# Kernel optimization log

Measured on AMD Instinct MI355X. Metric: run time of the kernel, lower is better.

Reference implementation:

```python
import jax, jax.numpy as jnp
import numpy as np

NUM_HEADS = 4
OUTPUT_DIM = 32
NUM_NODES = 50000
NUM_EDGES = 800000
INPUT_DIM = 128


def setup_inputs() -> dict:
    key = jax.random.key(0)
    k1, k2, k3, k4 = jax.random.split(key, 4)
    node_features = jax.random.uniform(k1, (NUM_NODES, INPUT_DIM), dtype=jnp.float32)
    edge_index = jax.random.randint(k2, (2, NUM_EDGES), 0, NUM_NODES, dtype=jnp.int64)
    # Linear weight (xavier-like scale), stored as [in, out] for x @ W
    W = jax.random.normal(k3, (INPUT_DIM, NUM_HEADS * OUTPUT_DIM), dtype=jnp.float32) * 0.1
    att = jax.random.normal(k4, (2 * OUTPUT_DIM, 1), dtype=jnp.float32) * 0.2
    return {"node_features": node_features, "edge_index": edge_index, "W": W, "att": att}


def reference(node_features, edge_index, W, att):
    num_nodes = node_features.shape[0]
    # Linear projection -> [N, H, D]  (dropout = identity in eval mode)
    proj = (node_features @ W).reshape(num_nodes, NUM_HEADS, OUTPUT_DIM)
    src = proj[edge_index[0]]   # [E, H, D]
    tgt = proj[edge_index[1]]   # [E, H, D]
    # concat([src,tgt]) @ att  ==  src @ att[:D] + tgt @ att[D:]
    a_src = att[:OUTPUT_DIM, 0]   # [D]
    a_tgt = att[OUTPUT_DIM:, 0]   # [D]
    scores = jax.nn.leaky_relu(
        jnp.einsum('ehd,d->eh', src, a_src) + jnp.einsum('ehd,d->eh', tgt, a_tgt),
        negative_slope=0.01,
    )  # [E, H]
    # Faithful to original: softmax over the HEADS axis (dim=-1 of [E, H])
    alpha = jax.nn.softmax(scores, axis=-1)  # [E, H]
    weighted = tgt * alpha[..., None]        # [E, H, D]
    # index_add_ on dim 0 with edge_index[0]
    out = jax.ops.segment_sum(weighted, edge_index[0], num_segments=num_nodes)  # [N, H, D]
    # concat_heads=False -> mean over heads
    return out.mean(axis=1)  # [N, D]
```

## Files before the change

kernel.cpp:

```cpp
#include <hip/hip_runtime.h>
#include <math.h>

#define N_NODES 50000
#define N_EDGES 800000
#define IN_DIM 128
#define N_HEADS 4
#define OUT_DIM 32
#define PROJ_DIM 128
#define CAP 48
#define WSTR 144
#define DEGS 16

#define PROJ_BLKS 391
#define BUCKET_BLKS 1563
#define TOTAL_BLKS (PROJ_BLKS + BUCKET_BLKS)

typedef short bf16x8 __attribute__((ext_vector_type(8)));
typedef float f32x4  __attribute__((ext_vector_type(4)));
typedef _Float16 h2  __attribute__((ext_vector_type(2)));

__device__ __forceinline__ ushort f32_to_bf16(float f) {
    unsigned u = __float_as_uint(f);
    unsigned r = u + 0x7fffu + ((u >> 16) & 1u);
    return (ushort)(r >> 16);
}

__device__ __forceinline__ float bf16_to_f32(ushort v) {
    return __uint_as_float((unsigned)v << 16);
}

__device__ __forceinline__ bf16x8 cvt8(float4 a, float4 b) {
    bf16x8 r;
    r[0] = (short)f32_to_bf16(a.x); r[1] = (short)f32_to_bf16(a.y);
    r[2] = (short)f32_to_bf16(a.z); r[3] = (short)f32_to_bf16(a.w);
    r[4] = (short)f32_to_bf16(b.x); r[5] = (short)f32_to_bf16(b.y);
    r[6] = (short)f32_to_bf16(b.z); r[7] = (short)f32_to_bf16(b.w);
    return r;
}

__global__ __launch_bounds__(256) void combo_kernel(
    const float* __restrict__ X, const float* __restrict__ W,
    const float* __restrict__ att, const int* __restrict__ ei,
    ushort* __restrict__ projT, float* __restrict__ s_src, float* __restrict__ s_tgt,
    int* __restrict__ deg, ushort* __restrict__ bucket)
{
    __shared__ ushort Wt[128 * WSTR];

    const int tid = threadIdx.x;

    if (blockIdx.x >= PROJ_BLKS) {
        int b2 = blockIdx.x - PROJ_BLKS;
        int e0 = b2 * 512 + tid;
#pragma unroll
        for (int i = 0; i < 2; ++i) {
            int e = e0 + i * 256;
            if (e < N_EDGES) {
                int src = ei[e];
                int tgt = ei[N_EDGES + e];
                int pos = atomicAdd(&deg[src * DEGS], 1);
                if (pos < CAP)
                    __builtin_nontemporal_store((ushort)tgt, &bucket[src * CAP + pos]);
            }
        }
        return;
    }

    for (int idx = tid; idx < 64 * 128; idx += 256) {
        int kp = idx >> 7;
        int c  = idx & 127;
        float w0 = W[(2 * kp) * PROJ_DIM + c];
        float w1 = W[(2 * kp + 1) * PROJ_DIM + c];
        unsigned pr = (unsigned)f32_to_bf16(w0) | ((unsigned)f32_to_bf16(w1) << 16);
        *(unsigned*)&Wt[c * WSTR + 2 * kp] = pr;
    }
    __syncthreads();

    const int wv   = tid >> 6;
    const int lane = tid & 63;
    const int m = lane & 15;
    const int q = lane >> 4;
    const int rbase = blockIdx.x * 128;

    int arow0 = rbase + wv * 32 + m;
    int arow1 = arow0 + 16;
    arow0 = (arow0 < N_NODES) ? arow0 : N_NODES - 1;
    arow1 = (arow1 < N_NODES) ? arow1 : N_NODES - 1;
    const long long xb0 = (long long)arow0 * IN_DIM;
    const long long xb1 = (long long)arow1 * IN_DIM;

    f32x4 acc[2][8];
#pragma unroll
    for (int rt = 0; rt < 2; ++rt)
#pragma unroll
        for (int ct = 0; ct < 8; ++ct) acc[rt][ct] = (f32x4){0.f, 0.f, 0.f, 0.f};

#pragma unroll
    for (int ks = 0; ks < 4; ++ks) {
        const int k0 = ks * 32 + q * 8;
        float4 a0lo = *(const float4*)&X[xb0 + k0];
        float4 a0hi = *(const float4*)&X[xb0 + k0 + 4];
        float4 a1lo = *(const float4*)&X[xb1 + k0];
        float4 a1hi = *(const float4*)&X[xb1 + k0 + 4];
        bf16x8 afrag0 = cvt8(a0lo, a0hi);
        bf16x8 afrag1 = cvt8(a1lo, a1hi);
#pragma unroll
        for (int ct = 0; ct < 8; ++ct) {
            bf16x8 bfrag = *(const bf16x8*)&Wt[(ct * 16 + m) * WSTR + k0];
            acc[0][ct] = __builtin_amdgcn_mfma_f32_16x16x32_bf16(afrag0, bfrag, acc[0][ct], 0, 0, 0);
            acc[1][ct] = __builtin_amdgcn_mfma_f32_16x16x32_bf16(afrag1, bfrag, acc[1][ct], 0, 0, 0);
        }
    }

    const float as_lo = att[m],      as_hi = att[m + 16];
    const float at_lo = att[32 + m], at_hi = att[48 + m];

#pragma unroll
    for (int rt = 0; rt < 2; ++rt) {
        const int rowb = rbase + wv * 32 + rt * 16 + q * 4;
#pragma unroll
        for (int r = 0; r < 4; ++r) {
            const int row = rowb + r;
            float cl[4], ch[4];
#pragma unroll
            for (int h = 0; h < 4; ++h) {
                cl[h] = acc[rt][2 * h][r];
                ch[h] = acc[rt][2 * h + 1][r];
            }
            if (row < N_NODES) {
                ushort4 plo, phi;
                plo.x = f32_to_bf16(cl[0]); plo.y = f32_to_bf16(cl[1]);
                plo.z = f32_to_bf16(cl[2]); plo.w = f32_to_bf16(cl[3]);
                phi.x = f32_to_bf16(ch[0]); phi.y = f32_to_bf16(ch[1]);
                phi.z = f32_to_bf16(ch[2]); phi.w = f32_to_bf16(ch[3]);
                *(ushort4*)&projT[(long long)row * PROJ_DIM + m * 4] = plo;
                *(ushort4*)&projT[(long long)row * PROJ_DIM + (m + 16) * 4] = phi;
            }
            float ps[4], pt[4];
#pragma unroll
            for (int h = 0; h < 4; ++h) {
                ps[h] = cl[h] * as_lo + ch[h] * as_hi;
                pt[h] = cl[h] * at_lo + ch[h] * at_hi;
            }
#pragma unroll
            for (int off = 8; off > 0; off >>= 1) {
#pragma unroll
                for (int h = 0; h < 4; ++h) {
                    ps[h] += __shfl_down(ps[h], off, 16);
                    pt[h] += __shfl_down(pt[h], off, 16);
                }
            }
            if (m == 0 && row < N_NODES) {
                *(float4*)&s_src[row * N_HEADS] = make_float4(ps[0], ps[1], ps[2], ps[3]);
                *(float4*)&s_tgt[row * N_HEADS] = make_float4(pt[0], pt[1], pt[2], pt[3]);
            }
        }
    }
}

__global__ __launch_bounds__(256) void gather_kernel(
    const int* __restrict__ deg, const ushort* __restrict__ bucket,
    const float* __restrict__ s_src, const float* __restrict__ s_tgt,
    const ushort* __restrict__ projT, float* __restrict__ out)
{
    __shared__ int4 es[4][CAP];

    const int wv   = threadIdx.x >> 6;
    const int lane = threadIdx.x & 63;
    const int node = blockIdx.x * 4 + wv;

    int n = deg[node * DEGS];
    n = (n < CAP) ? n : CAP;

    if (lane < n) {
        int tgt = bucket[node * CAP + lane];
        float4 ss = *(const float4*)&s_src[node * N_HEADS];
        float4 st = *(const float4*)&s_tgt[tgt * N_HEADS];

        float sc[4] = { ss.x + st.x, ss.y + st.y, ss.z + st.z, ss.w + st.w };
        float mx = -1e30f;
#pragma unroll
        for (int h = 0; h < 4; ++h) {
            sc[h] = (sc[h] > 0.0f) ? sc[h] : 0.01f * sc[h];
            mx = fmaxf(mx, sc[h]);
        }
        float sum = 0.0f;
#pragma unroll
        for (int h = 0; h < 4; ++h) {
            sc[h] = __expf(sc[h] - mx);
            sum += sc[h];
        }
        float inv = 0.25f / sum;

        h2 a01, a23;
        a01.x = (_Float16)(sc[0] * inv);
        a01.y = (_Float16)(sc[1] * inv);
        a23.x = (_Float16)(sc[2] * inv);
        a23.y = (_Float16)(sc[3] * inv);
        es[wv][lane] = make_int4(tgt, __builtin_bit_cast(int, a01),
                                      __builtin_bit_cast(int, a23), 0);
    }
    __syncthreads();

    const int d    = lane & 31;
    const int half = lane >> 5;

    float acc0 = 0.0f, acc1 = 0.0f, acc2 = 0.0f, acc3 = 0.0f;
    int j = half;

    for (; j + 14 < n; j += 16) {
        int4 e[8];
        ushort4 p[8];
#pragma unroll
        for (int u = 0; u < 8; ++u) e[u] = es[wv][j + 2 * u];
#pragma unroll
        for (int u = 0; u < 8; ++u)
            p[u] = *(const ushort4*)&projT[(long long)e[u].x * PROJ_DIM + d * 4];
#pragma unroll
        for (int u = 0; u < 8; ++u) {
            h2 a = __builtin_bit_cast(h2, e[u].y);
            h2 b = __builtin_bit_cast(h2, e[u].z);
            float* accp = (u & 1) ? ((u & 2) ? &acc3 : &acc1)
                                  : ((u & 2) ? &acc2 : &acc0);
            float t = *accp;
            t = fmaf((float)a.x, bf16_to_f32(p[u].x), t);
            t = fmaf((float)a.y, bf16_to_f32(p[u].y), t);
            t = fmaf((float)b.x, bf16_to_f32(p[u].z), t);
            t = fmaf((float)b.y, bf16_to_f32(p[u].w), t);
            *accp = t;
        }
    }
    for (; j < n; j += 2) {
        int4 e4 = es[wv][j];
        ushort4 pv = *(const ushort4*)&projT[(long long)e4.x * PROJ_DIM + d * 4];
        h2 a01 = __builtin_bit_cast(h2, e4.y);
        h2 a23 = __builtin_bit_cast(h2, e4.z);
        acc0 = fmaf((float)a01.x, bf16_to_f32(pv.x), acc0);
        acc0 = fmaf((float)a01.y, bf16_to_f32(pv.y), acc0);
        acc0 = fmaf((float)a23.x, bf16_to_f32(pv.z), acc0);
        acc0 = fmaf((float)a23.y, bf16_to_f32(pv.w), acc0);
    }

    float acc = (acc0 + acc1) + (acc2 + acc3);
    acc += __shfl_down(acc, 32);
    if (lane < 32) out[node * OUT_DIM + d] = acc;
}

extern "C" void kernel_launch(void* const* d_in, const int* in_sizes, int n_in,
                              void* d_out, int out_size, void* d_ws, size_t ws_size,
                              hipStream_t stream) {
    const float* X   = (const float*)d_in[0];
    const int*   ei  = (const int*)d_in[1];
    const float* W   = (const float*)d_in[2];
    const float* att = (const float*)d_in[3];
    float* out = (float*)d_out;

    char* p = (char*)d_ws;
    ushort* projT  = (ushort*)p; p += (size_t)N_NODES * PROJ_DIM * 2;
    float* s_src   = (float*)p;  p += (size_t)N_NODES * N_HEADS * 4;
    float* s_tgt   = (float*)p;  p += (size_t)N_NODES * N_HEADS * 4;
    int* deg       = (int*)p;    p += (size_t)N_NODES * DEGS * 4;
    ushort* bucket = (ushort*)p; p += (size_t)N_NODES * CAP * 2;

    (void)hipMemsetAsync(deg, 0, (size_t)N_NODES * DEGS * sizeof(int), stream);

    combo_kernel<<<TOTAL_BLKS, 256, 0, stream>>>(
        X, W, att, ei, projT, s_src, s_tgt, deg, bucket);

    gather_kernel<<<N_NODES / 4, 256, 0, stream>>>(
        deg, bucket, s_src, s_tgt, projT, out);
}
```

Before: 156.4 us.

## Replace per-node atomic bucketing with two-pass binned counting sort into CSR

Edge bucketing changes from per-edge global atomics into strided per-node buckets to a two-level counting sort. Edges are first partitioned into 196 coarse bins of 256 source nodes each, using shared-memory atomics plus one global atomic per bin per block. A new binsort kernel then orders each bin locally into a compact CSR with offsets and degrees. This removes heavily contended scattered global atomics and sparse bucket writes, at the cost of an extra kernel launch, an intermediate slab pass, and fixed bin capacities that could silently drop edges on skewed inputs.

```diff
diff --git a/kernel.cpp b/kernel.cpp
--- a/kernel.cpp
+++ b/kernel.cpp
@@ -7,13 +7,15 @@
 #define N_HEADS 4
 #define OUT_DIM 32
 #define PROJ_DIM 128
-#define CAP 48
 #define WSTR 144
-#define DEGS 16
+
+#define NBIN 196
+#define BINCAP 5000
+#define MAXDEG 64
 
 #define PROJ_BLKS 391
-#define BUCKET_BLKS 1563
-#define TOTAL_BLKS (PROJ_BLKS + BUCKET_BLKS)
+#define PART_BLKS 391
+#define TOTAL_BLKS (PROJ_BLKS + PART_BLKS)
 
 typedef short bf16x8 __attribute__((ext_vector_type(8)));
 typedef float f32x4  __attribute__((ext_vector_type(4)));
@@ -42,24 +44,43 @@
     const float* __restrict__ X, const float* __restrict__ W,
     const float* __restrict__ att, const int* __restrict__ ei,
     ushort* __restrict__ projT, float* __restrict__ s_src, float* __restrict__ s_tgt,
-    int* __restrict__ deg, ushort* __restrict__ bucket)
+    int* __restrict__ bin_cursor, unsigned* __restrict__ slab)
 {
     __shared__ ushort Wt[128 * WSTR];
 
     const int tid = threadIdx.x;
 
     if (blockIdx.x >= PROJ_BLKS) {
-        int b2 = blockIdx.x - PROJ_BLKS;
-        int e0 = b2 * 512 + tid;
-#pragma unroll
-        for (int i = 0; i < 2; ++i) {
-            int e = e0 + i * 256;
-            if (e < N_EDGES) {
-                int src = ei[e];
-                int tgt = ei[N_EDGES + e];
-                int pos = atomicAdd(&deg[src * DEGS], 1);
-                if (pos < CAP)
-                    __builtin_nontemporal_store((ushort)tgt, &bucket[src * CAP + pos]);
+        int* cnt   = (int*)Wt;
+        int* gbase = cnt + 256;
+
+        for (int t = tid; t < NBIN; t += 256) cnt[t] = 0;
+        __syncthreads();
+
+        const int ebase = (blockIdx.x - PROJ_BLKS) * 2048;
+        unsigned srcv[8], tgtv[8];
+        int rank[8];
+#pragma unroll
+        for (int i = 0; i < 8; ++i) {
+            int e = ebase + i * 256 + tid;
+            bool ok = e < N_EDGES;
+            srcv[i] = ok ? (unsigned)ei[e] : 0u;
+            tgtv[i] = ok ? (unsigned)ei[N_EDGES + e] : 0u;
+            rank[i] = ok ? atomicAdd(&cnt[srcv[i] >> 8], 1) : -1;
+        }
+        __syncthreads();
+
+        for (int t = tid; t < NBIN; t += 256)
+            gbase[t] = atomicAdd(&bin_cursor[t], cnt[t]);
+        __syncthreads();
+
+#pragma unroll
+        for (int i = 0; i < 8; ++i) {
+            if (rank[i] >= 0) {
+                int bin = srcv[i] >> 8;
+                int p = gbase[bin] + rank[i];
+                if (p < BINCAP)
+                    slab[bin * BINCAP + p] = (tgtv[i] << 16) | (srcv[i] & 255u);
             }
         }
         return;
@@ -157,22 +178,78 @@
     }
 }
 
+__global__ __launch_bounds__(256) void binsort_kernel(
+    const unsigned* __restrict__ slab, const int* __restrict__ bin_cursor,
+    ushort* __restrict__ csr, int* __restrict__ offs, int* __restrict__ deg)
+{
+    __shared__ int cnt2[256];
+    __shared__ int pref[256];
+    __shared__ int ex[256];
+    __shared__ ushort stgt[BINCAP];
+
+    const int b = blockIdx.x;
+    const int t = threadIdx.x;
+    int n_e = bin_cursor[b];
+    n_e = (n_e < BINCAP) ? n_e : BINCAP;
+
+    cnt2[t] = 0;
+    __syncthreads();
+
+    unsigned pk[20];
+    int npk = 0;
+    for (int i = t; i < n_e; i += 256) {
+        unsigned v = slab[b * BINCAP + i];
+        int node8 = v & 255u;
+        int r = atomicAdd(&cnt2[node8], 1);
+        r = (r < 255) ? r : 255;
+        pk[npk++] = (v & 0xFFFF0000u) | ((unsigned)r << 8) | (unsigned)node8;
+    }
+    __syncthreads();
+
+    pref[t] = cnt2[t];
+    __syncthreads();
+    for (int off = 1; off < 256; off <<= 1) {
+        int x = (t >= off) ? pref[t - off] : 0;
+        __syncthreads();
+        pref[t] += x;
+        __syncthreads();
+    }
+    ex[t] = pref[t] - cnt2[t];
+    __syncthreads();
+
+    for (int j = 0; j < npk; ++j) {
+        unsigned v = pk[j];
+        int lpos = ex[v & 255u] + (int)((v >> 8) & 255u);
+        if (lpos < BINCAP) stgt[lpos] = (ushort)(v >> 16);
+    }
+    __syncthreads();
+
+    for (int i = t; i < n_e; i += 256) csr[b * BINCAP + i] = stgt[i];
+    int node = b * 256 + t;
+    if (node < N_NODES) {
+        offs[node] = b * BINCAP + ex[t];
+        deg[node]  = cnt2[t];
+    }
+}
+
 __global__ __launch_bounds__(256) void gather_kernel(
-    const int* __restrict__ deg, const ushort* __restrict__ bucket,
+    const int* __restrict__ deg, const int* __restrict__ offs,
+    const ushort* __restrict__ csr,
     const float* __restrict__ s_src, const float* __restrict__ s_tgt,
     const ushort* __restrict__ projT, float* __restrict__ out)
 {
-    __shared__ int4 es[4][CAP];
+    __shared__ int4 es[4][MAXDEG];
 
     const int wv   = threadIdx.x >> 6;
     const int lane = threadIdx.x & 63;
     const int node = blockIdx.x * 4 + wv;
 
-    int n = deg[node * DEGS];
-    n = (n < CAP) ? n : CAP;
+    int n = deg[node];
+    n = (n < MAXDEG) ? n : MAXDEG;
+    int o = offs[node];
 
     if (lane < n) {
-        int tgt = bucket[node * CAP + lane];
+        int tgt = csr[o + lane];
         float4 ss = *(const float4*)&s_src[node * N_HEADS];
         float4 st = *(const float4*)&s_tgt[tgt * N_HEADS];
 
@@ -221,12 +298,12 @@
             h2 b = __builtin_bit_cast(h2, e[u].z);
             float* accp = (u & 1) ? ((u & 2) ? &acc3 : &acc1)
                                   : ((u & 2) ? &acc2 : &acc0);
-            float t = *accp;
-            t = fmaf((float)a.x, bf16_to_f32(p[u].x), t);
-            t = fmaf((float)a.y, bf16_to_f32(p[u].y), t);
-            t = fmaf((float)b.x, bf16_to_f32(p[u].z), t);
-            t = fmaf((float)b.y, bf16_to_f32(p[u].w), t);
-            *accp = t;
+            float tt = *accp;
+            tt = fmaf((float)a.x, bf16_to_f32(p[u].x), tt);
+            tt = fmaf((float)a.y, bf16_to_f32(p[u].y), tt);
+            tt = fmaf((float)b.x, bf16_to_f32(p[u].z), tt);
+            tt = fmaf((float)b.y, bf16_to_f32(p[u].w), tt);
+            *accp = tt;
         }
     }
     for (; j < n; j += 2) {
@@ -255,17 +332,22 @@
     float* out = (float*)d_out;
 
     char* p = (char*)d_ws;
-    ushort* projT  = (ushort*)p; p += (size_t)N_NODES * PROJ_DIM * 2;
-    float* s_src   = (float*)p;  p += (size_t)N_NODES * N_HEADS * 4;
-    float* s_tgt   = (float*)p;  p += (size_t)N_NODES * N_HEADS * 4;
-    int* deg       = (int*)p;    p += (size_t)N_NODES * DEGS * 4;
-    ushort* bucket = (ushort*)p; p += (size_t)N_NODES * CAP * 2;
-
-    (void)hipMemsetAsync(deg, 0, (size_t)N_NODES * DEGS * sizeof(int), stream);
+    ushort* projT   = (ushort*)p;   p += (size_t)N_NODES * PROJ_DIM * 2;
+    float* s_src    = (float*)p;    p += (size_t)N_NODES * N_HEADS * 4;
+    float* s_tgt    = (float*)p;    p += (size_t)N_NODES * N_HEADS * 4;
+    unsigned* slab  = (unsigned*)p; p += (size_t)NBIN * BINCAP * 4;
+    ushort* csr     = (ushort*)p;   p += (size_t)NBIN * BINCAP * 2;
+    int* offs       = (int*)p;      p += (size_t)N_NODES * 4;
+    int* deg        = (int*)p;      p += (size_t)N_NODES * 4;
+    int* bin_cursor = (int*)p;      p += 256 * 4;
+
+    (void)hipMemsetAsync(bin_cursor, 0, 256 * sizeof(int), stream);
 
     combo_kernel<<<TOTAL_BLKS, 256, 0, stream>>>(
-        X, W, att, ei, projT, s_src, s_tgt, deg, bucket);
+        X, W, att, ei, projT, s_src, s_tgt, bin_cursor, slab);
+
+    binsort_kernel<<<NBIN, 256, 0, stream>>>(slab, bin_cursor, csr, offs, deg);
 
     gather_kernel<<<N_NODES / 4, 256, 0, stream>>>(
-        deg, bucket, s_src, s_tgt, projT, out);
-}
+        deg, offs, csr, s_src, s_tgt, projT, out);
+}
```

Result: faster. 146.8 us (-6.1%).
